# Optimization experiments

Hardware: AMD Instinct MI355X
Metric: run time of the kernel (lower is better)

The kernel has to match this reference:

```python
import jax, jax.numpy as jnp
import numpy as np

# Config (mirrors init_kwargs)
IN_FEATURES = 1024
N_CLASSES = 50257
CUTOFFS = [4000, 20000, 50257]   # cutoffs + [n_classes]
SHORTLIST = 4000
N_CLUSTERS = 2
HEAD_SIZE = SHORTLIST + N_CLUSTERS  # 4002
HSZ = [IN_FEATURES // 4, IN_FEATURES // 16]   # div_value**1, div_value**2 -> 256, 64
OSZ = [CUTOFFS[1] - CUTOFFS[0], CUTOFFS[2] - CUTOFFS[1]]  # 16000, 30257
N = 4096


def setup_inputs() -> dict:
    key = jax.random.key(0)
    ks = jax.random.split(key, 8)
    s = 0.02
    return {
        "myinput": jax.random.normal(ks[0], (N, IN_FEATURES), dtype=jnp.float32),
        "target": jax.random.randint(ks[1], (N,), 0, N_CLASSES),
        # head Linear (bias=False): weight stored as [in, out]
        "head_W": (jax.random.normal(ks[2], (IN_FEATURES, HEAD_SIZE), dtype=jnp.float32) * s),
        # tail cluster 0: Linear(in, 256, bias=False) -> Linear(256, 16000, bias=False)
        "t0_W1": (jax.random.normal(ks[3], (IN_FEATURES, HSZ[0]), dtype=jnp.float32) * s),
        "t0_W2": (jax.random.normal(ks[4], (HSZ[0], OSZ[0]), dtype=jnp.float32) * s),
        # tail cluster 1: Linear(in, 64, bias=False) -> Linear(64, 30257, bias=False)
        "t1_W1": (jax.random.normal(ks[5], (IN_FEATURES, HSZ[1]), dtype=jnp.float32) * s),
        "t1_W2": (jax.random.normal(ks[6], (HSZ[1], OSZ[1]), dtype=jnp.float32) * s),
    }


def _cluster_logprob(x, target, W1, W2, lo, hi, mask):
    # low-rank tail projection for one cluster, computed densely over all rows
    # then masked by membership (same math as the torch gather/scatter dispatch).
    logits = (x @ W1) @ W2                       # [N, osz]
    rel = jnp.clip(target - lo, 0, hi - lo - 1)  # in-range dummy for non-members
    picked = jnp.take_along_axis(logits, rel[:, None], axis=1)[:, 0]
    lp = picked - jax.nn.logsumexp(logits, axis=1)  # log_softmax gathered at rel
    return jnp.where(mask, lp, jnp.float32(0.0))


def reference(myinput, target, head_W, t0_W1, t0_W2, t1_W1, t1_W2):
    # Dropout (tail_drop) is identity in eval mode.
    in0 = (target >= CUTOFFS[0]) & (target < CUTOFFS[1])
    in1 = target >= CUTOFFS[1]
    # gather index into head: raw target for shortlist, cluster token otherwise
    gather_inds = jnp.where(in0, SHORTLIST, jnp.where(in1, SHORTLIST + 1, target))
    head_lp = jax.nn.log_softmax(myinput @ head_W, axis=-1)   # [N, 4002]
    out = jnp.take_along_axis(head_lp, gather_inds[:, None], axis=1)[:, 0]
    out = out + _cluster_logprob(myinput, target, t0_W1, t0_W2, CUTOFFS[0], CUTOFFS[1], in0)
    out = out + _cluster_logprob(myinput, target, t1_W1, t1_W2, CUTOFFS[1], CUTOFFS[2], in1)
    loss = -jnp.mean(out)
    return out, loss
```

## Files before the change

### kernel.cpp

```cpp
#include <hip/hip_runtime.h>
#include <hip/hip_bf16.h>
#include <math.h>
#include <stdint.h>

#define N_ROWS 4096
#define IN_F   1024
#define HEAD_N 4002
#define C0_H   256
#define C0_N   16000
#define C1_H   64
#define C1_N   30257
#define CUT0   4000
#define CUT1   20000
#define HW1    384

#define LOG2E 1.4426950408889634f
#define LN2   0.6931471805599453f

typedef __attribute__((ext_vector_type(8))) short bf16x8;
typedef __attribute__((ext_vector_type(4))) float f32x4;

__device__ __forceinline__ float exp2_fast(float x) {
    return __builtin_amdgcn_exp2f(x);
}

__device__ __forceinline__ ushort f2bf(float f) {
    uint32_t u = __builtin_bit_cast(uint32_t, f);
    uint32_t r = (u + 0x7fffu + ((u >> 16) & 1u)) >> 16;
    return (ushort)r;
}
__device__ __forceinline__ float bf2f(ushort u) {
    return __builtin_bit_cast(float, (uint32_t)u << 16);
}

__device__ __forceinline__ void gload_lds_16(const void* gsrc, void* ldst) {
    __builtin_amdgcn_global_load_lds(
        (const __attribute__((address_space(1))) void*)(uintptr_t)gsrc,
        (__attribute__((address_space(3))) void*)(uint32_t)(uintptr_t)ldst,
        16, 0, 0);
}

__global__ __launch_bounds__(256)
void cast_f32_bf16(const float* __restrict__ in, ushort* __restrict__ out, int n)
{
    int i = (blockIdx.x * 256 + threadIdx.x) * 4;
    if (i >= n) return;
    float4 v = *reinterpret_cast<const float4*>(in + i);
    ushort4 o;
    o.x = f2bf(v.x); o.y = f2bf(v.y); o.z = f2bf(v.z); o.w = f2bf(v.w);
    *reinterpret_cast<ushort4*>(out + i) = o;
}

__global__ __launch_bounds__(256)
void castT(const float* __restrict__ B, ushort* __restrict__ BT, int K, int N,
           float scale)
{
    __shared__ float t[32][33];
    const int tx = threadIdx.x, ty = threadIdx.y;
    const int n0 = blockIdx.x * 32, k0 = blockIdx.y * 32;
    #pragma unroll
    for (int i = 0; i < 4; ++i) {
        int n = n0 + tx;
        t[ty + i * 8][tx] = (n < N) ? B[(size_t)(k0 + ty + i * 8) * N + n] : 0.0f;
    }
    __syncthreads();
    #pragma unroll
    for (int i = 0; i < 4; ++i) {
        int n = n0 + ty + i * 8;
        BT[(size_t)n * K + k0 + tx] = f2bf(t[tx][ty + i * 8] * scale);
    }
}

__global__ __launch_bounds__(256)
void gemm_out(const ushort* __restrict__ A, int lda,
              const ushort* __restrict__ BT, int ldb, int K,
              int Nreal, ushort* __restrict__ Cout, int ldc)
{
    __shared__ ushort As[128 * 32];
    __shared__ ushort Bs[128 * 32];
    const int tid = threadIdx.x;
    const int l = tid & 63, w = tid >> 6;
    const int rowBase = blockIdx.y * 128, colBase = blockIdx.x * 128;
    const int rsel = l & 15, ksel = l >> 4;
    const int sr = l >> 2, skq = (l & 3) * 8;

    f32x4 acc[2][8];
    #pragma unroll
    for (int mi = 0; mi < 2; ++mi)
        #pragma unroll
        for (int ni = 0; ni < 8; ++ni) acc[mi][ni] = (f32x4){0.f, 0.f, 0.f, 0.f};

    for (int k0 = 0; k0 < K; k0 += 32) {
        #pragma unroll
        for (int i = 0; i < 2; ++i) {
            const int c = w + i * 4;
            gload_lds_16(A + (size_t)(rowBase + c * 16 + sr) * lda + k0 + skq,
                         (char*)As + c * 1024);
            gload_lds_16(BT + (size_t)(colBase + c * 16 + sr) * ldb + k0 + skq,
                         (char*)Bs + c * 1024);
        }
        __syncthreads();
        bf16x8 af[2], bfr[8];
        #pragma unroll
        for (int mi = 0; mi < 2; ++mi)
            af[mi] = *reinterpret_cast<const bf16x8*>(As + (w * 32 + mi * 16 + rsel) * 32 + ksel * 8);
        #pragma unroll
        for (int ni = 0; ni < 8; ++ni)
            bfr[ni] = *reinterpret_cast<const bf16x8*>(Bs + (ni * 16 + rsel) * 32 + ksel * 8);
        #pragma unroll
        for (int mi = 0; mi < 2; ++mi)
            #pragma unroll
            for (int ni = 0; ni < 8; ++ni)
                acc[mi][ni] = __builtin_amdgcn_mfma_f32_16x16x32_bf16(af[mi], bfr[ni], acc[mi][ni], 0, 0, 0);
        __syncthreads();
    }
    #pragma unroll
    for (int mi = 0; mi < 2; ++mi)
        #pragma unroll
        for (int ni = 0; ni < 8; ++ni) {
            const int col = colBase + ni * 16 + rsel;
            if (col < Nreal) {
                #pragma unroll
                for (int j = 0; j < 4; ++j) {
                    const int row = rowBase + w * 32 + mi * 16 + ksel * 4 + j;
                    Cout[(size_t)row * ldc + col] = f2bf(acc[mi][ni][j]);
                }
            }
        }
}

__global__ __launch_bounds__(256, 4)
void sumexp_pipe(const ushort* __restrict__ A, int lda,
                 const ushort* __restrict__ BT, int ldb,
                 int K, int nCT, int ntiles, int Nreal,
                 float* __restrict__ ps, int nsplit)
{
    __shared__ ushort As[2][128 * 32];
    __shared__ ushort Bs[2][128 * 32];

    const int id = blockIdx.x;
    const int xsplit = ((id >> 8) << 3) + (id & 7);
    const int yrow   = (id & 255) >> 3;

    const int tid = threadIdx.x;
    const int l = tid & 63, w = tid >> 6;
    const int rowBase = yrow * 128;
    const int rsel = l & 15, ksel = l >> 4;

    const int kchunks = K >> 5;
    const int ct0 = xsplit * ntiles;
    const int ctn = min(ntiles, nCT - ct0);
    const int nch = ctn * kchunks;

    const int srow = l >> 2;
    const int skq = ((((l & 3) << 4) ^ ((srow & 3) << 4)) >> 1);

    f32x4 acc[2][8];
    float s_run[2][4];
    #pragma unroll
    for (int mi = 0; mi < 2; ++mi)
        #pragma unroll
        for (int j = 0; j < 4; ++j) s_run[mi][j] = 0.f;

    int i_kh = 0, i_ct = 0, issued = 0;
    #define ISSUE()                                                            \
    do {                                                                       \
        const int buf = issued & 1;                                            \
        const int k0 = i_kh << 5;                                              \
        const size_t cb = (size_t)(ct0 + i_ct) << 7;                           \
        _Pragma("unroll")                                                      \
        for (int i = 0; i < 2; ++i) {                                          \
            const int c = w + i * 4;                                           \
            const int row = c * 16 + srow;                                     \
            gload_lds_16(A + (size_t)(rowBase + row) * lda + k0 + skq,         \
                         (char*)&As[buf][0] + c * 1024);                       \
            gload_lds_16(BT + (cb + row) * ldb + k0 + skq,                     \
                         (char*)&Bs[buf][0] + c * 1024);                       \
        }                                                                      \
        ++issued;                                                              \
        if (++i_kh == kchunks) { i_kh = 0; ++i_ct; }                           \
    } while (0)

    ISSUE();
    if (nch > 1) ISSUE();

    const int swz = (rsel & 3) << 3;
    int c_kh = 0;
    int c_colBase = ct0 << 7;

    for (int ch = 0; ch < nch; ++ch) {
        if (ch + 1 < nch) asm volatile("s_waitcnt vmcnt(4)" ::: "memory");
        else              asm volatile("s_waitcnt vmcnt(0)" ::: "memory");
        __builtin_amdgcn_s_barrier();

        if (c_kh == 0) {
            #pragma unroll
            for (int mi = 0; mi < 2; ++mi)
                #pragma unroll
                for (int ni = 0; ni < 8; ++ni)
                    acc[mi][ni] = (f32x4){0.f, 0.f, 0.f, 0.f};
        }

        const int buf = ch & 1;
        bf16x8 af[2], bfr[8];
        #pragma unroll
        for (int mi = 0; mi < 2; ++mi)
            af[mi] = *reinterpret_cast<const bf16x8*>(
                &As[buf][(w * 32 + mi * 16 + rsel) * 32 + ((ksel * 8) ^ swz)]);
        #pragma unroll
        for (int ni = 0; ni < 8; ++ni)
            bfr[ni] = *reinterpret_cast<const bf16x8*>(
                &Bs[buf][(ni * 16 + rsel) * 32 + ((ksel * 8) ^ swz)]);
        #pragma unroll
        for (int mi = 0; mi < 2; ++mi)
            #pragma unroll
            for (int ni = 0; ni < 8; ++ni)
                acc[mi][ni] = __builtin_amdgcn_mfma_f32_16x16x32_bf16(
                    af[mi], bfr[ni], acc[mi][ni], 0, 0, 0);

        __builtin_amdgcn_s_barrier();
        if (issued < nch) ISSUE();

        if (c_kh == kchunks - 1) {
            if (c_colBase + 128 > Nreal) {
                #pragma unroll
                for (int mi = 0; mi < 2; ++mi)
                    #pragma unroll
                    for (int ni = 0; ni < 8; ++ni) {
                        const bool ok = (c_colBase + ni * 16 + rsel) < Nreal;
                        #pragma unroll
                        for (int j = 0; j < 4; ++j)
                            s_run[mi][j] += ok ? exp2_fast(acc[mi][ni][j]) : 0.f;
                    }
            } else {
                #pragma unroll
                for (int mi = 0; mi < 2; ++mi)
                    #pragma unroll
                    for (int ni = 0; ni < 8; ++ni)
                        #pragma unroll
                        for (int j = 0; j < 4; ++j)
                            s_run[mi][j] += exp2_fast(acc[mi][ni][j]);
            }
            c_kh = 0;
            c_colBase += 128;
        } else {
            ++c_kh;
        }
    }
    #undef ISSUE

    #pragma unroll
    for (int mi = 0; mi < 2; ++mi)
        #pragma unroll
        for (int j = 0; j < 4; ++j) {
            float S = s_run[mi][j];
            #pragma unroll
            for (int off = 8; off; off >>= 1) S += __shfl_xor(S, off);
            if (rsel == 0) {
                const int row = rowBase + w * 32 + mi * 16 + ksel * 4 + j;
                ps[(size_t)row * nsplit + xsplit] = S;
            }
        }
}

__global__ __launch_bounds__(256)
void gather_dot(const ushort* __restrict__ x_bf,
                const ushort* __restrict__ h_comb,
                const ushort* __restrict__ headWT,
                const ushort* __restrict__ t0W2T,
                const ushort* __restrict__ t1W2T,
                const int* __restrict__ target,
                float* __restrict__ pk_h, float* __restrict__ pk_c)
{
    const int r = blockIdx.x * 4 + (threadIdx.x >> 6);
    const int l = threadIdx.x & 63;
    const int t = target[r];

    const int gh = (t < CUT0) ? t : ((t < CUT1) ? CUT0 : CUT0 + 1);
    const ushort* xr = x_bf + (size_t)r * IN_F + l * 16;
    const ushort* wr = headWT + (size_t)gh * IN_F + l * 16;
    float s = 0.f;
    #pragma unroll
    for (int v = 0; v < 2; ++v) {
        ushort4 xa = *reinterpret_cast<const ushort4*>(xr + v * 8);
        ushort4 xb = *reinterpret_cast<const ushort4*>(xr + v * 8 + 4);
        ushort4 wa = *reinterpret_cast<const ushort4*>(wr + v * 8);
        ushort4 wb = *reinterpret_cast<const ushort4*>(wr + v * 8 + 4);
        s += bf2f(xa.x) * bf2f(wa.x) + bf2f(xa.y) * bf2f(wa.y)
           + bf2f(xa.z) * bf2f(wa.z) + bf2f(xa.w) * bf2f(wa.w)
           + bf2f(xb.x) * bf2f(wb.x) + bf2f(xb.y) * bf2f(wb.y)
           + bf2f(xb.z) * bf2f(wb.z) + bf2f(xb.w) * bf2f(wb.w);
    }
    #pragma unroll
    for (int off = 32; off; off >>= 1) s += __shfl_xor(s, off);
    if (l == 0) pk_h[r] = s * LN2;

    if (t >= CUT0) {
        float c = 0.f;
        if (t < CUT1) {
            const ushort* hr = h_comb + (size_t)r * HW1 + l * 4;
            const ushort* vr = t0W2T + (size_t)(t - CUT0) * C0_H + l * 4;
            ushort4 ha = *reinterpret_cast<const ushort4*>(hr);
            ushort4 va = *reinterpret_cast<const ushort4*>(vr);
            c = bf2f(ha.x) * bf2f(va.x) + bf2f(ha.y) * bf2f(va.y)
              + bf2f(ha.z) * bf2f(va.z) + bf2f(ha.w) * bf2f(va.w);
        } else {
            c = bf2f(h_comb[(size_t)r * HW1 + C0_H + l]) *
                bf2f(t1W2T[(size_t)(t - CUT1) * C1_H + l]);
        }
        #pragma unroll
        for (int off = 32; off; off >>= 1) c += __shfl_xor(c, off);
        if (l == 0) pk_c[r] = c * LN2;
    }
}

__global__ __launch_bounds__(256)
void combine_rows(const float* __restrict__ ps_h, const float* __restrict__ ps_0,
                  const float* __restrict__ ps_1,
                  const float* __restrict__ pk_h, const float* __restrict__ pk_c,
                  const int* __restrict__ target, float* __restrict__ out,
                  int ns_h, int ns_0, int ns_1)
{
    const int r = blockIdx.x * 256 + threadIdx.x;
    if (r >= N_ROWS) return;
    float S = 0.f;
    const float* p = ps_h + (size_t)r * ns_h;
    for (int i = 0; i < ns_h; ++i) S += p[i];
    float o = pk_h[r] - __logf(S);
    const int t = target[r];
    if (t >= CUT0) {
        const float* q; int n;
        if (t < CUT1) { q = ps_0 + (size_t)r * ns_0; n = ns_0; }
        else          { q = ps_1 + (size_t)r * ns_1; n = ns_1; }
        float S2 = 0.f;
        for (int i = 0; i < n; ++i) S2 += q[i];
        o += pk_c[r] - __logf(S2);
    }
    out[r] = o;
}

__global__ __launch_bounds__(256)
void finalize_loss(const float* __restrict__ out, float* __restrict__ loss)
{
    float s = 0.f;
    for (int r = threadIdx.x; r < N_ROWS; r += 256) s += out[r];
    #pragma unroll
    for (int off = 32; off; off >>= 1) s += __shfl_xor(s, off);
    __shared__ float red[4];
    if ((threadIdx.x & 63) == 0) red[threadIdx.x >> 6] = s;
    __syncthreads();
    if (threadIdx.x == 0)
        loss[0] = -(red[0] + red[1] + red[2] + red[3]) / (float)N_ROWS;
}

extern "C" void kernel_launch(void* const* d_in, const int* in_sizes, int n_in,
                              void* d_out, int out_size, void* d_ws, size_t ws_size,
                              hipStream_t stream)
{
    const float* x      = (const float*)d_in[0];
    const int*   target = (const int*)  d_in[1];
    const float* head_W = (const float*)d_in[2];
    const float* t0_W1  = (const float*)d_in[3];
    const float* t0_W2  = (const float*)d_in[4];
    const float* t1_W1  = (const float*)d_in[5];
    const float* t1_W2  = (const float*)d_in[6];
    float* out = (float*)d_out;

    const int HPAD  = 4096;
    const int C0PAD = 16000;
    const int C1PAD = 30336;
    const int nCT_h = HPAD / 128;
    const int nCT_0 = C0PAD / 128;
    const int nCT_1 = C1PAD / 128;

    const int NT_H = 2,  NS_H = 16;
    const int NT_0 = 4,  NS_0 = 32;
    const int NT_1 = 6,  NS_1 = 40;

    ushort* us = (ushort*)d_ws;
    ushort* x_bf   = us; us += (size_t)N_ROWS * IN_F;
    ushort* headWT = us; us += (size_t)HPAD * IN_F;
    ushort* hW1T   = us; us += (size_t)HW1 * IN_F;
    ushort* t0W2T  = us; us += (size_t)C0PAD * C0_H;
    ushort* t1W2T  = us; us += (size_t)C1PAD * C1_H;
    ushort* h_comb = us; us += (size_t)N_ROWS * HW1;

    float* ws   = (float*)us;
    float* ps_h = ws; ws += (size_t)N_ROWS * NS_H;
    float* ps_0 = ws; ws += (size_t)N_ROWS * NS_0;
    float* ps_1 = ws; ws += (size_t)N_ROWS * NS_1;
    float* pk_h = ws; ws += N_ROWS;
    float* pk_c = ws; ws += N_ROWS;

    const dim3 blk(256);

    hipLaunchKernelGGL(cast_f32_bf16, dim3(N_ROWS * IN_F / 1024), blk, 0, stream,
                       x, x_bf, N_ROWS * IN_F);
    hipLaunchKernelGGL(castT, dim3(HPAD / 32, IN_F / 32), dim3(32, 8), 0, stream,
                       head_W, headWT, IN_F, HEAD_N, LOG2E);
    hipLaunchKernelGGL(castT, dim3(C0_H / 32, IN_F / 32), dim3(32, 8), 0, stream,
                       t0_W1, hW1T, IN_F, C0_H, 1.0f);
    hipLaunchKernelGGL(castT, dim3(128 / 32, IN_F / 32), dim3(32, 8), 0, stream,
                       t1_W1, hW1T + (size_t)C0_H * IN_F, IN_F, C1_H, 1.0f);
    hipLaunchKernelGGL(castT, dim3(C0PAD / 32, C0_H / 32), dim3(32, 8), 0, stream,
                       t0_W2, t0W2T, C0_H, C0_N, LOG2E);
    hipLaunchKernelGGL(castT, dim3(C1PAD / 32, C1_H / 32), dim3(32, 8), 0, stream,
                       t1_W2, t1W2T, C1_H, C1_N, LOG2E);

    hipLaunchKernelGGL(gemm_out, dim3(HW1 / 128, N_ROWS / 128), blk, 0, stream,
                       x_bf, IN_F, hW1T, IN_F, IN_F, C0_H + C1_H, h_comb, HW1);

    hipLaunchKernelGGL(sumexp_pipe, dim3(NS_H * 32), blk, 0, stream,
                       x_bf, IN_F, headWT, IN_F, IN_F, nCT_h, NT_H, HEAD_N, ps_h, NS_H);
    hipLaunchKernelGGL(sumexp_pipe, dim3(NS_0 * 32), blk, 0, stream,
                       h_comb, HW1, t0W2T, C0_H, C0_H, nCT_0, NT_0, C0_N, ps_0, NS_0);
    hipLaunchKernelGGL(sumexp_pipe, dim3(NS_1 * 32), blk, 0, stream,
                       h_comb + C0_H, HW1, t1W2T, C1_H, C1_H, nCT_1, NT_1, C1_N, ps_1, NS_1);

    hipLaunchKernelGGL(gather_dot, dim3(N_ROWS / 4), blk, 0, stream,
                       x_bf, h_comb, headWT, t0W2T, t1W2T, target, pk_h, pk_c);
    hipLaunchKernelGGL(combine_rows, dim3(N_ROWS / 256), blk, 0, stream,
                       ps_h, ps_0, ps_1, pk_h, pk_c, target, out, NS_H, NS_0, NS_1);
    hipLaunchKernelGGL(finalize_loss, dim3(1), blk, 0, stream, out, out + N_ROWS);
}
```

Baseline: 194.8 us.

## Enlarge sumexp GEMM tile to 128x256 with 64x128 per-wave subtiles

The fused matmul+sum-exp kernel moves from a 128x128 block tile with 32x128 per-wave tiles to a 128x256 tile where each wave computes a 64x128 subtile. This doubles the accumulator registers, lowers occupancy to 2 blocks per SIMD-group, and combines the two column halves through a small shared-memory reduction. Padding and split counts change to match 256-column tiles. The aim is higher arithmetic intensity per LDS read and per global load, at the cost of register pressure and fewer resident waves.

```diff
diff --git a/kernel.cpp b/kernel.cpp
--- a/kernel.cpp
+++ b/kernel.cpp
@@ -129,14 +129,15 @@
         }
 }
 
-__global__ __launch_bounds__(256, 4)
+__global__ __launch_bounds__(256, 2)
 void sumexp_pipe(const ushort* __restrict__ A, int lda,
                  const ushort* __restrict__ BT, int ldb,
                  int K, int nCT, int ntiles, int Nreal,
                  float* __restrict__ ps, int nsplit)
 {
     __shared__ ushort As[2][128 * 32];
-    __shared__ ushort Bs[2][128 * 32];
+    __shared__ ushort Bs[2][256 * 32];
+    __shared__ float sred[128];
 
     const int id = blockIdx.x;
     const int xsplit = ((id >> 8) << 3) + (id & 7);
@@ -155,10 +156,14 @@
     const int srow = l >> 2;
     const int skq = ((((l & 3) << 4) ^ ((srow & 3) << 4)) >> 1);
 
-    f32x4 acc[2][8];
-    float s_run[2][4];
-    #pragma unroll
-    for (int mi = 0; mi < 2; ++mi)
+    const int wrow = (w >> 1) * 64;
+    const int wcol = (w & 1) * 128;
+    const int koff = (ksel * 8) ^ ((rsel & 3) << 3);
+
+    f32x4 acc[4][8];
+    float s_run[4][4];
+    #pragma unroll
+    for (int mi = 0; mi < 4; ++mi)
         #pragma unroll
         for (int j = 0; j < 4; ++j) s_run[mi][j] = 0.f;
 
@@ -167,14 +172,17 @@
     do {                                                                       \
         const int buf = issued & 1;                                            \
         const int k0 = i_kh << 5;                                              \
-        const size_t cb = (size_t)(ct0 + i_ct) << 7;                           \
+        const size_t cb = (size_t)(ct0 + i_ct) << 8;                           \
         _Pragma("unroll")                                                      \
-        for (int i = 0; i < 2; ++i) {                                          \
-            const int c = w + i * 4;                                           \
-            const int row = c * 16 + srow;                                     \
-            gload_lds_16(A + (size_t)(rowBase + row) * lda + k0 + skq,         \
+        for (int i = 0; i < 2; ++i) {      \
+            const int c = w * 2 + i;                                           \
+            gload_lds_16(A + (size_t)(rowBase + c * 16 + srow) * lda + k0 + skq,\
                          (char*)&As[buf][0] + c * 1024);                       \
-            gload_lds_16(BT + (cb + row) * ldb + k0 + skq,                     \
+        }                                                                      \
+        _Pragma("unroll")                                                      \
+        for (int i = 0; i < 4; ++i) {    \
+            const int c = w * 4 + i;                                           \
+            gload_lds_16(BT + (cb + c * 16 + srow) * ldb + k0 + skq,           \
                          (char*)&Bs[buf][0] + c * 1024);                       \
         }                                                                      \
         ++issued;                                                              \
@@ -184,35 +192,34 @@
     ISSUE();
     if (nch > 1) ISSUE();
 
-    const int swz = (rsel & 3) << 3;
     int c_kh = 0;
-    int c_colBase = ct0 << 7;
+    int c_colBase = ct0 << 8;
 
     for (int ch = 0; ch < nch; ++ch) {
-        if (ch + 1 < nch) asm volatile("s_waitcnt vmcnt(4)" ::: "memory");
+        if (ch + 1 < nch) asm volatile("s_waitcnt vmcnt(6)" ::: "memory");
         else              asm volatile("s_waitcnt vmcnt(0)" ::: "memory");
         __builtin_amdgcn_s_barrier();
 
         if (c_kh == 0) {
             #pragma unroll
-            for (int mi = 0; mi < 2; ++mi)
+            for (int mi = 0; mi < 4; ++mi)
                 #pragma unroll
                 for (int ni = 0; ni < 8; ++ni)
                     acc[mi][ni] = (f32x4){0.f, 0.f, 0.f, 0.f};
         }
 
         const int buf = ch & 1;
-        bf16x8 af[2], bfr[8];
-        #pragma unroll
-        for (int mi = 0; mi < 2; ++mi)
+        bf16x8 af[4], bfr[8];
+        #pragma unroll
+        for (int mi = 0; mi < 4; ++mi)
             af[mi] = *reinterpret_cast<const bf16x8*>(
-                &As[buf][(w * 32 + mi * 16 + rsel) * 32 + ((ksel * 8) ^ swz)]);
+                &As[buf][(wrow + mi * 16 + rsel) * 32 + koff]);
         #pragma unroll
         for (int ni = 0; ni < 8; ++ni)
             bfr[ni] = *reinterpret_cast<const bf16x8*>(
-                &Bs[buf][(ni * 16 + rsel) * 32 + ((ksel * 8) ^ swz)]);
-        #pragma unroll
-        for (int mi = 0; mi < 2; ++mi)
+                &Bs[buf][(wcol + ni * 16 + rsel) * 32 + koff]);
+        #pragma unroll
+        for (int mi = 0; mi < 4; ++mi)
             #pragma unroll
             for (int ni = 0; ni < 8; ++ni)
                 acc[mi][ni] = __builtin_amdgcn_mfma_f32_16x16x32_bf16(
@@ -222,19 +229,20 @@
         if (issued < nch) ISSUE();
 
         if (c_kh == kchunks - 1) {
-            if (c_colBase + 128 > Nreal) {
+            const int cbase = c_colBase + wcol;
+            if (cbase + 128 > Nreal) {
                 #pragma unroll
-                for (int mi = 0; mi < 2; ++mi)
+                for (int ni = 0; ni < 8; ++ni) {
+                    const bool ok = (cbase + ni * 16 + rsel) < Nreal;
                     #pragma unroll
-                    for (int ni = 0; ni < 8; ++ni) {
-                        const bool ok = (c_colBase + ni * 16 + rsel) < Nreal;
+                    for (int mi = 0; mi < 4; ++mi)
                         #pragma unroll
                         for (int j = 0; j < 4; ++j)
                             s_run[mi][j] += ok ? exp2_fast(acc[mi][ni][j]) : 0.f;
-                    }
+                }
             } else {
                 #pragma unroll
-                for (int mi = 0; mi < 2; ++mi)
+                for (int mi = 0; mi < 4; ++mi)
                     #pragma unroll
                     for (int ni = 0; ni < 8; ++ni)
                         #pragma unroll
@@ -242,7 +250,7 @@
                             s_run[mi][j] += exp2_fast(acc[mi][ni][j]);
             }
             c_kh = 0;
-            c_colBase += 128;
+            c_colBase += 256;
         } else {
             ++c_kh;
         }
@@ -250,17 +258,27 @@
     #undef ISSUE
 
     #pragma unroll
-    for (int mi = 0; mi < 2; ++mi)
+    for (int mi = 0; mi < 4; ++mi)
         #pragma unroll
         for (int j = 0; j < 4; ++j) {
             float S = s_run[mi][j];
             #pragma unroll
             for (int off = 8; off; off >>= 1) S += __shfl_xor(S, off);
-            if (rsel == 0) {
-                const int row = rowBase + w * 32 + mi * 16 + ksel * 4 + j;
-                ps[(size_t)row * nsplit + xsplit] = S;
+            s_run[mi][j] = S;
+            if ((w & 1) == 1 && rsel == 0)
+                sred[wrow + mi * 16 + ksel * 4 + j] = S;
+        }
+    __syncthreads();
+    if ((w & 1) == 0 && rsel == 0) {
+        #pragma unroll
+        for (int mi = 0; mi < 4; ++mi)
+            #pragma unroll
+            for (int j = 0; j < 4; ++j) {
+                const int lrow = wrow + mi * 16 + ksel * 4 + j;
+                ps[(size_t)(rowBase + lrow) * nsplit + xsplit] =
+                    s_run[mi][j] + sred[lrow];
             }
-        }
+    }
 }
 
 __global__ __launch_bounds__(256)
@@ -367,15 +385,15 @@
     float* out = (float*)d_out;
 
     const int HPAD  = 4096;
-    const int C0PAD = 16000;
-    const int C1PAD = 30336;
-    const int nCT_h = HPAD / 128;
-    const int nCT_0 = C0PAD / 128;
-    const int nCT_1 = C1PAD / 128;
-
-    const int NT_H = 2,  NS_H = 16;
-    const int NT_0 = 4,  NS_0 = 32;
-    const int NT_1 = 6,  NS_1 = 40;
+    const int C0PAD = 16128;
+    const int C1PAD = 30464;
+    const int nCT_h = HPAD / 256;
+    const int nCT_0 = C0PAD / 256;
+    const int nCT_1 = C1PAD / 256;
+
+    const int NT_H = 2,  NS_H = 8;
+    const int NT_0 = 4,  NS_0 = 16;
+    const int NT_1 = 5,  NS_1 = 24;
 
     ushort* us = (ushort*)d_ws;
     ushort* x_bf   = us; us += (size_t)N_ROWS * IN_F;
```

Result: no change. 197.1 us (+1.2%).

## Merge prep casts, sumexp GEMMs, and gather/combine into fewer launches

Applied to the files above, without the earlier changes.

Folds the six cast and transpose kernels into one prep kernel, and the three sumexp GEMM launches into one grid that branches on block index. It also fuses gather_dot with combine_rows, so each row's partial sums are reduced by wave shuffles and the output is written directly. The head split changes from 2 tiles over 16 splits to 1 tile over 32 splits. The goal is to cut launch overhead and tail idle time between dependent launches, at the cost of a divergent, heterogeneous block mix in the merged kernels.

```diff
diff --git a/kernel.cpp b/kernel.cpp
--- a/kernel.cpp
+++ b/kernel.cpp
@@ -17,6 +17,22 @@
 #define LOG2E 1.4426950408889634f
 #define LN2   0.6931471805599453f
 
+#define HPAD   4096
+#define C0PAD  16000
+#define C1PAD  30336
+#define NCT_H  32
+#define NCT_0  125
+#define NCT_1  237
+#define NT_H   1
+#define NT_0   4
+#define NT_1   6
+#define NS_H   32
+#define NS_0   32
+#define NS_1   40
+#define GRID_H (NS_H * 32)
+#define GRID_0 (NS_0 * 32)
+#define GRID_1 (NS_1 * 32)
+
 typedef __attribute__((ext_vector_type(8))) short bf16x8;
 typedef __attribute__((ext_vector_type(4))) float f32x4;
 
@@ -40,24 +56,13 @@
         16, 0, 0);
 }
 
-__global__ __launch_bounds__(256)
-void cast_f32_bf16(const float* __restrict__ in, ushort* __restrict__ out, int n)
-{
-    int i = (blockIdx.x * 256 + threadIdx.x) * 4;
-    if (i >= n) return;
-    float4 v = *reinterpret_cast<const float4*>(in + i);
-    ushort4 o;
-    o.x = f2bf(v.x); o.y = f2bf(v.y); o.z = f2bf(v.z); o.w = f2bf(v.w);
-    *reinterpret_cast<ushort4*>(out + i) = o;
-}
-
-__global__ __launch_bounds__(256)
-void castT(const float* __restrict__ B, ushort* __restrict__ BT, int K, int N,
-           float scale)
-{
-    __shared__ float t[32][33];
-    const int tx = threadIdx.x, ty = threadIdx.y;
-    const int n0 = blockIdx.x * 32, k0 = blockIdx.y * 32;
+__device__ __forceinline__ void castT_body(const float* __restrict__ B,
+                                           ushort* __restrict__ BT,
+                                           int K, int N, float scale,
+                                           int n0, int k0, int tid,
+                                           float (*t)[33])
+{
+    const int tx = tid & 31, ty = tid >> 5;
     #pragma unroll
     for (int i = 0; i < 4; ++i) {
         int n = n0 + tx;
@@ -68,6 +73,57 @@
     for (int i = 0; i < 4; ++i) {
         int n = n0 + ty + i * 8;
         BT[(size_t)n * K + k0 + tx] = f2bf(t[tx][ty + i * 8] * scale);
+    }
+}
+
+__global__ __launch_bounds__(256)
+void prep(const float* __restrict__ x, ushort* __restrict__ x_bf,
+          const float* __restrict__ head_W, ushort* __restrict__ headWT,
+          const float* __restrict__ t0_W1, const float* __restrict__ t1_W1,
+          ushort* __restrict__ hW1T,
+          const float* __restrict__ t0_W2, ushort* __restrict__ t0W2T,
+          const float* __restrict__ t1_W2, ushort* __restrict__ t1W2T)
+{
+    __shared__ float t[32][33];
+    const int tid = threadIdx.x;
+    int id = blockIdx.x;
+
+    if (id < 4096) {
+        int i = (id * 256 + tid) * 4;
+        float4 v = *reinterpret_cast<const float4*>(x + i);
+        ushort4 o;
+        o.x = f2bf(v.x); o.y = f2bf(v.y); o.z = f2bf(v.z); o.w = f2bf(v.w);
+        *reinterpret_cast<ushort4*>(x_bf + i) = o;
+        return;
+    }
+    id -= 4096;
+    if (id < 4096) {
+        castT_body(head_W, headWT, IN_F, HEAD_N, LOG2E,
+                   (id % 128) * 32, (id / 128) * 32, tid, t);
+        return;
+    }
+    id -= 4096;
+    if (id < 256) {
+        castT_body(t0_W1, hW1T, IN_F, C0_H, 1.0f,
+                   (id % 8) * 32, (id / 8) * 32, tid, t);
+        return;
+    }
+    id -= 256;
+    if (id < 128) {
+        castT_body(t1_W1, hW1T + (size_t)C0_H * IN_F, IN_F, C1_H, 1.0f,
+                   (id % 4) * 32, (id / 4) * 32, tid, t);
+        return;
+    }
+    id -= 128;
+    if (id < 4000) {
+        castT_body(t0_W2, t0W2T, C0_H, C0_N, LOG2E,
+                   (id % 500) * 32, (id / 500) * 32, tid, t);
+        return;
+    }
+    id -= 4000;
+    {
+        castT_body(t1_W2, t1W2T, C1_H, C1_N, LOG2E,
+                   (id % 948) * 32, (id / 948) * 32, tid, t);
     }
 }
 
@@ -129,18 +185,15 @@
         }
 }
 
-__global__ __launch_bounds__(256, 4)
-void sumexp_pipe(const ushort* __restrict__ A, int lda,
-                 const ushort* __restrict__ BT, int ldb,
-                 int K, int nCT, int ntiles, int Nreal,
-                 float* __restrict__ ps, int nsplit)
-{
-    __shared__ ushort As[2][128 * 32];
-    __shared__ ushort Bs[2][128 * 32];
-
-    const int id = blockIdx.x;
-    const int xsplit = ((id >> 8) << 3) + (id & 7);
-    const int yrow   = (id & 255) >> 3;
+__device__ __forceinline__ void sumexp_body(
+    const ushort* __restrict__ A, int lda,
+    const ushort* __restrict__ BT, int ldb,
+    int K, int nCT, int ntiles, int Nreal,
+    float* __restrict__ ps, int nsplit, int lid,
+    ushort (*As)[128 * 32], ushort (*Bs)[128 * 32])
+{
+    const int xsplit = ((lid >> 8) << 3) + (lid & 7);
+    const int yrow   = (lid & 255) >> 3;
 
     const int tid = threadIdx.x;
     const int l = tid & 63, w = tid >> 6;
@@ -263,14 +316,40 @@
         }
 }
 
+__global__ __launch_bounds__(256, 4)
+void sumexp3(const ushort* __restrict__ x_bf, const ushort* __restrict__ h_comb,
+             const ushort* __restrict__ headWT, const ushort* __restrict__ t0W2T,
+             const ushort* __restrict__ t1W2T,
+             float* __restrict__ ps_h, float* __restrict__ ps_0,
+             float* __restrict__ ps_1)
+{
+    __shared__ ushort As[2][128 * 32];
+    __shared__ ushort Bs[2][128 * 32];
+
+    const int id = blockIdx.x;
+    if (id < GRID_H) {
+        sumexp_body(x_bf, IN_F, headWT, IN_F, IN_F, NCT_H, NT_H, HEAD_N,
+                    ps_h, NS_H, id, As, Bs);
+    } else if (id < GRID_H + GRID_0) {
+        sumexp_body(h_comb, HW1, t0W2T, C0_H, C0_H, NCT_0, NT_0, C0_N,
+                    ps_0, NS_0, id - GRID_H, As, Bs);
+    } else {
+        sumexp_body(h_comb + C0_H, HW1, t1W2T, C1_H, C1_H, NCT_1, NT_1, C1_N,
+                    ps_1, NS_1, id - GRID_H - GRID_0, As, Bs);
+    }
+}
+
 __global__ __launch_bounds__(256)
-void gather_dot(const ushort* __restrict__ x_bf,
-                const ushort* __restrict__ h_comb,
-                const ushort* __restrict__ headWT,
-                const ushort* __restrict__ t0W2T,
-                const ushort* __restrict__ t1W2T,
-                const int* __restrict__ target,
-                float* __restrict__ pk_h, float* __restrict__ pk_c)
+void gather_combine(const ushort* __restrict__ x_bf,
+                    const ushort* __restrict__ h_comb,
+                    const ushort* __restrict__ headWT,
+                    const ushort* __restrict__ t0W2T,
+                    const ushort* __restrict__ t1W2T,
+                    const int* __restrict__ target,
+                    const float* __restrict__ ps_h,
+                    const float* __restrict__ ps_0,
+                    const float* __restrict__ ps_1,
+                    float* __restrict__ out)
 {
     const int r = blockIdx.x * 4 + (threadIdx.x >> 6);
     const int l = threadIdx.x & 63;
@@ -293,7 +372,12 @@
     }
     #pragma unroll
     for (int off = 32; off; off >>= 1) s += __shfl_xor(s, off);
-    if (l == 0) pk_h[r] = s * LN2;
+
+    float Sh = (l < NS_H) ? ps_h[(size_t)r * NS_H + l] : 0.f;
+    #pragma unroll
+    for (int off = 32; off; off >>= 1) Sh += __shfl_xor(Sh, off);
+
+    float o = s * LN2 - __logf(Sh);
 
     if (t >= CUT0) {
         float c = 0.f;
@@ -310,33 +394,16 @@
         }
         #pragma unroll
         for (int off = 32; off; off >>= 1) c += __shfl_xor(c, off);
-        if (l == 0) pk_c[r] = c * LN2;
-    }
-}
-
-__global__ __launch_bounds__(256)
-void combine_rows(const float* __restrict__ ps_h, const float* __restrict__ ps_0,
-                  const float* __restrict__ ps_1,
-                  const float* __restrict__ pk_h, const float* __restrict__ pk_c,
-                  const int* __restrict__ target, float* __restrict__ out,
-                  int ns_h, int ns_0, int ns_1)
-{
-    const int r = blockIdx.x * 256 + threadIdx.x;
-    if (r >= N_ROWS) return;
-    float S = 0.f;
-    const float* p = ps_h + (size_t)r * ns_h;
-    for (int i = 0; i < ns_h; ++i) S += p[i];
-    float o = pk_h[r] - __logf(S);
-    const int t = target[r];
-    if (t >= CUT0) {
-        const float* q; int n;
-        if (t < CUT1) { q = ps_0 + (size_t)r * ns_0; n = ns_0; }
-        else          { q = ps_1 + (size_t)r * ns_1; n = ns_1; }
-        float S2 = 0.f;
-        for (int i = 0; i < n; ++i) S2 += q[i];
-        o += pk_c[r] - __logf(S2);
-    }
-    out[r] = o;
+
+        float Sc;
+        if (t < CUT1) Sc = (l < NS_0) ? ps_0[(size_t)r * NS_0 + l] : 0.f;
+        else          Sc = (l < NS_1) ? ps_1[(size_t)r * NS_1 + l] : 0.f;
+        #pragma unroll
+        for (int off = 32; off; off >>= 1) Sc += __shfl_xor(Sc, off);
+
+        o += c * LN2 - __logf(Sc);
+    }
+    if (l == 0) out[r] = o;
 }
 
 __global__ __launch_bounds__(256)
@@ -366,17 +433,6 @@
     const float* t1_W2  = (const float*)d_in[6];
     float* out = (float*)d_out;
 
-    const int HPAD  = 4096;
-    const int C0PAD = 16000;
-    const int C1PAD = 30336;
-    const int nCT_h = HPAD / 128;
-    const int nCT_0 = C0PAD / 128;
-    const int nCT_1 = C1PAD / 128;
-
-    const int NT_H = 2,  NS_H = 16;
-    const int NT_0 = 4,  NS_0 = 32;
-    const int NT_1 = 6,  NS_1 = 40;
-
     ushort* us = (ushort*)d_ws;
     ushort* x_bf   = us; us += (size_t)N_ROWS * IN_F;
     ushort* headWT = us; us += (size_t)HPAD * IN_F;
@@ -389,37 +445,21 @@
     float* ps_h = ws; ws += (size_t)N_ROWS * NS_H;
     float* ps_0 = ws; ws += (size_t)N_ROWS * NS_0;
     float* ps_1 = ws; ws += (size_t)N_ROWS * NS_1;
-    float* pk_h = ws; ws += N_ROWS;
-    float* pk_c = ws; ws += N_ROWS;
 
     const dim3 blk(256);
 
-    hipLaunchKernelGGL(cast_f32_bf16, dim3(N_ROWS * IN_F / 1024), blk, 0, stream,
-                       x, x_bf, N_ROWS * IN_F);
-    hipLaunchKernelGGL(castT, dim3(HPAD / 32, IN_F / 32), dim3(32, 8), 0, stream,
-                       head_W, headWT, IN_F, HEAD_N, LOG2E);
-    hipLaunchKernelGGL(castT, dim3(C0_H / 32, IN_F / 32), dim3(32, 8), 0, stream,
-                       t0_W1, hW1T, IN_F, C0_H, 1.0f);
-    hipLaunchKernelGGL(castT, dim3(128 / 32, IN_F / 32), dim3(32, 8), 0, stream,
-                       t1_W1, hW1T + (size_t)C0_H * IN_F, IN_F, C1_H, 1.0f);
-    hipLaunchKernelGGL(castT, dim3(C0PAD / 32, C0_H / 32), dim3(32, 8), 0, stream,
-                       t0_W2, t0W2T, C0_H, C0_N, LOG2E);
-    hipLaunchKernelGGL(castT, dim3(C1PAD / 32, C1_H / 32), dim3(32, 8), 0, stream,
-                       t1_W2, t1W2T, C1_H, C1_N, LOG2E);
+    hipLaunchKernelGGL(prep, dim3(14472), blk, 0, stream,
+                       x, x_bf, head_W, headWT, t0_W1, t1_W1, hW1T,
+                       t0_W2, t0W2T, t1_W2, t1W2T);
 
     hipLaunchKernelGGL(gemm_out, dim3(HW1 / 128, N_ROWS / 128), blk, 0, stream,
                        x_bf, IN_F, hW1T, IN_F, IN_F, C0_H + C1_H, h_comb, HW1);
 
-    hipLaunchKernelGGL(sumexp_pipe, dim3(NS_H * 32), blk, 0, stream,
-                       x_bf, IN_F, headWT, IN_F, IN_F, nCT_h, NT_H, HEAD_N, ps_h, NS_H);
-    hipLaunchKernelGGL(sumexp_pipe, dim3(NS_0 * 32), blk, 0, stream,
-                       h_comb, HW1, t0W2T, C0_H, C0_H, nCT_0, NT_0, C0_N, ps_0, NS_0);
-    hipLaunchKernelGGL(sumexp_pipe, dim3(NS_1 * 32), blk, 0, stream,
-                       h_comb + C0_H, HW1, t1W2T, C1_H, C1_H, nCT_1, NT_1, C1_N, ps_1, NS_1);
-
-    hipLaunchKernelGGL(gather_dot, dim3(N_ROWS / 4), blk, 0, stream,
-                       x_bf, h_comb, headWT, t0W2T, t1W2T, target, pk_h, pk_c);
-    hipLaunchKernelGGL(combine_rows, dim3(N_ROWS / 256), blk, 0, stream,
-                       ps_h, ps_0, ps_1, pk_h, pk_c, target, out, NS_H, NS_0, NS_1);
+    hipLaunchKernelGGL(sumexp3, dim3(GRID_H + GRID_0 + GRID_1), blk, 0, stream,
+                       x_bf, h_comb, headWT, t0W2T, t1W2T, ps_h, ps_0, ps_1);
+
+    hipLaunchKernelGGL(gather_combine, dim3(N_ROWS / 4), blk, 0, stream,
+                       x_bf, h_comb, headWT, t0W2T, t1W2T, target,
+                       ps_h, ps_0, ps_1, out);
     hipLaunchKernelGGL(finalize_loss, dim3(1), blk, 0, stream, out, out + N_ROWS);
 }
```

Result: slower. 258.4 us (+32.6%).
